# Kernel optimization log

Hardware: AMD Instinct MI355X
Metric: run time of the kernel (lower is better)

## Reference

```python
import jax, jax.numpy as jnp
import numpy as np

N = 4
SEGMENTS = 16
IN_F = 256
OUT_F = 256
BATCH = 512


def chebyshev_lobatto(n):
    # Chebyshev-Lobatto interpolation nodes on [-1, 1]
    k = jnp.arange(n, dtype=jnp.float32)
    return -jnp.cos(jnp.pi * k / (n - 1))


def lagrange_basis(x, nodes):
    # x: [B, In]; returns basis values [B, In, n]
    n = nodes.shape[0]
    cols = []
    for j in range(n):  # n is a small static constant (4)
        terms = [(x - nodes[m]) / (nodes[j] - nodes[m]) for m in range(n) if m != j]
        cols.append(jnp.prod(jnp.stack(terms, axis=0), axis=0))
    return jnp.stack(cols, axis=-1)


def setup_inputs() -> dict:
    key = jax.random.key(0)
    k1, k2 = jax.random.split(key)
    x = jax.random.uniform(k1, (BATCH, IN_F), dtype=jnp.float32, minval=-1.0, maxval=1.0)
    w = jax.random.uniform(
        k2, (OUT_F, IN_F, (N - 1) * SEGMENTS + 1), dtype=jnp.float32, minval=-1.0, maxval=1.0
    )
    return {"x": x, "w": w, "n": N, "segments": SEGMENTS}


def reference(x, w, n, segments):
    nodes = chebyshev_lobatto(n)
    # segment id per element, clamped to [0, segments-1]
    id_min = jnp.clip(((x + 1.0) / 2.0 * segments).astype(jnp.int32), 0, segments - 1)
    id_max = id_min + 1
    wid_min = id_min * (n - 1)  # start of weight slice; slice length == n
    # segment boundaries in x-space: eta(i) = i/segments * 2 - 1
    x_min = id_min.astype(x.dtype) / segments * 2.0 - 1.0
    x_max = id_max.astype(x.dtype) / segments * 2.0 - 1.0
    # rescale x into [-1, 1] within its segment
    x_in = 2.0 * (x - x_min) / (x_max - x_min) - 1.0
    basis = lagrange_basis(x_in, nodes)  # [B, In, n]
    # gather per-element weight slice: w_g[b,i,j,o] = w[o, i, wid_min[b,i]+j]
    idx = wid_min[..., None] + jnp.arange(n)  # [B, In, n]
    w_t = jnp.transpose(w, (1, 2, 0))  # [In, K, Out]
    in_f = w.shape[1]
    w_g = w_t[jnp.arange(in_f)[None, :, None], idx]  # [B, In, n, Out]
    # interpolate and sum over in_features (matches einsum 'ijk,jkli->jl')
    return jnp.einsum("bin,bino->bo", basis, w_g)
```

## Files before the change

kernel.cpp:

```cpp
#include <hip/hip_runtime.h>


typedef _Float16 h2 __attribute__((ext_vector_type(2)));

#define INF     256
#define OUTF    256
#define WSTRIDE 49
#define OSTRIDE (INF * WSTRIDE)
#define NSPLIT  32
#define IPB     8
#define WE_UINTS (256 * 128 * 64)

#define GLOAD16(gptr, lptr)                                                         \
  __builtin_amdgcn_global_load_lds(                                                 \
      (const __attribute__((address_space(1))) unsigned int*)(gptr),                \
      (__attribute__((address_space(3))) unsigned int*)(lptr), 16, 0, 0)

__global__ __launch_bounds__(256)
void pp_expand(const float* __restrict__ w, unsigned int* __restrict__ we) {
    const int i = blockIdx.x;
    const int o = threadIdx.x;
    const float* src = w + (size_t)o * OSTRIDE + i * WSTRIDE;
    float t[49];
    #pragma unroll
    for (int k = 0; k < 49; ++k) t[k] = src[k];
    const int op = o >> 1, e = o & 1;
    unsigned int* dst = we + ((size_t)i * 128 + op) * 64 + e * 2;
    #pragma unroll
    for (int s = 0; s < 16; ++s) {
        auto p0 = __builtin_amdgcn_cvt_pkrtz(t[3*s],   t[3*s+1]);
        auto p1 = __builtin_amdgcn_cvt_pkrtz(t[3*s+2], t[3*s+3]);
        uint2 v;
        v.x = __builtin_bit_cast(unsigned int, p0);
        v.y = __builtin_bit_cast(unsigned int, p1);
        *(uint2*)(dst + s * 4) = v;
    }
}

__global__ __launch_bounds__(256, 4)
void pp_partial(const float* __restrict__ x, const unsigned int* __restrict__ we,
                float* __restrict__ part) {
    __shared__ unsigned int smem[8192];

    const int tid  = threadIdx.x;
    const int wave = tid >> 6, lane = tid & 63;
    const int isplit  = blockIdx.x;
    const int i_base  = isplit * IPB;
    const int op_base = blockIdx.y * 16;
    const int o_base  = blockIdx.y * 32;
    const int b_base  = blockIdx.z * 64;
    const int b = b_base + lane;

    #pragma unroll
    for (int it = 0; it < 8; ++it) {
        int u = it * 256 + tid;
        int iloc = u >> 8, opl = (u >> 4) & 15, s = u & 15;
        const unsigned int* gp =
            we + (((size_t)(i_base + iloc) * 128 + op_base + opl) * 16 + s) * 4;
        GLOAD16(gp, &smem[u * 4]);
    }

    int sseg[IPB]; h2 cA[IPB], cB[IPB];
    {
        const float4* xp = (const float4*)(x + (size_t)b * INF + i_base);
        float4 x0 = xp[0], x1 = xp[1];
        float xs[8] = {x0.x, x0.y, x0.z, x0.w, x1.x, x1.y, x1.z, x1.w};
        #pragma unroll
        for (int i = 0; i < IPB; ++i) {
            float xx = xs[i];
            int id = (int)((xx + 1.0f) * 8.0f);
            id = id < 0 ? 0 : (id > 15 ? 15 : id);
            float u = (xx - ((float)id * 0.125f - 1.0f)) * 16.0f - 1.0f;
            float a = u + 1.0f, b2 = u + 0.5f, cc = u - 0.5f, d = u - 1.0f;
            float c0 = b2 * cc * d  * (-2.0f / 3.0f);
            float c1 = a  * cc * d  * ( 4.0f / 3.0f);
            float c2 = a  * b2 * d  * (-4.0f / 3.0f);
            float c3 = a  * b2 * cc * ( 2.0f / 3.0f);
            h2 pA; pA[0] = (_Float16)c0; pA[1] = (_Float16)c1;
            h2 pB; pB[0] = (_Float16)c2; pB[1] = (_Float16)c3;
            cA[i] = pA; cB[i] = pB; sseg[i] = id;
        }
    }

    __syncthreads();

    float acc[8];
    #pragma unroll
    for (int q = 0; q < 8; ++q) acc[q] = 0.0f;

    #pragma unroll
    for (int i = 0; i < IPB; ++i) {
        const unsigned int* p = &smem[(i * 16 + wave * 4) * 64 + sseg[i] * 4];
        #pragma unroll
        for (int pq = 0; pq < 4; ++pq) {
            uint4 v = *(const uint4*)(p + pq * 64);
            acc[2*pq]   = __builtin_amdgcn_fdot2(__builtin_bit_cast(h2, v.x), cA[i],
                                                 acc[2*pq],   false);
            acc[2*pq]   = __builtin_amdgcn_fdot2(__builtin_bit_cast(h2, v.y), cB[i],
                                                 acc[2*pq],   false);
            acc[2*pq+1] = __builtin_amdgcn_fdot2(__builtin_bit_cast(h2, v.z), cA[i],
                                                 acc[2*pq+1], false);
            acc[2*pq+1] = __builtin_amdgcn_fdot2(__builtin_bit_cast(h2, v.w), cB[i],
                                                 acc[2*pq+1], false);
        }
    }

    __syncthreads();
    float* smf = (float*)smem;
    #pragma unroll
    for (int q = 0; q < 8; ++q)
        smf[lane * 33 + wave * 8 + q] = acc[q];
    __syncthreads();

    const int qo = tid & 7;
    const int g  = tid >> 3;
    #pragma unroll
    for (int r = 0; r < 2; ++r) {
        int b_l = g + 32 * r;
        float4 v;
        v.x = smf[b_l * 33 + qo * 4 + 0];
        v.y = smf[b_l * 33 + qo * 4 + 1];
        v.z = smf[b_l * 33 + qo * 4 + 2];
        v.w = smf[b_l * 33 + qo * 4 + 3];
        *(float4*)(part + (size_t)isplit * (512 * 256)
                        + (size_t)(b_base + b_l) * 256 + o_base + qo * 4) = v;
    }
}

__global__ __launch_bounds__(256)
void pp_reduce(const float* __restrict__ part, float* __restrict__ out) {
    const size_t off4 = (size_t)blockIdx.x * 256 + threadIdx.x;
    const float4* p4 = (const float4*)part;
    float4 s = make_float4(0.f, 0.f, 0.f, 0.f);
    #pragma unroll
    for (int k = 0; k < NSPLIT; ++k) {
        float4 v = p4[(size_t)k * (512 * 64) + off4];
        s.x += v.x; s.y += v.y; s.z += v.z; s.w += v.w;
    }
    ((float4*)out)[off4] = s;
}

extern "C" void kernel_launch(void* const* d_in, const int* in_sizes, int n_in,
                              void* d_out, int out_size, void* d_ws, size_t ws_size,
                              hipStream_t stream) {
    const float* x = (const float*)d_in[0];
    const float* w = (const float*)d_in[1];
    float* out = (float*)d_out;
    unsigned int* we = (unsigned int*)d_ws;
    float* part = (float*)((char*)d_ws + (size_t)WE_UINTS * 4);
    (void)ws_size; (void)n_in; (void)in_sizes; (void)out_size;

    pp_expand<<<dim3(256), 256, 0, stream>>>(w, we);
    pp_partial<<<dim3(NSPLIT, 8, 8), 256, 0, stream>>>(x, we, part);
    pp_reduce<<<dim3(128), 256, 0, stream>>>(part, out);
}
```

Baseline: 86.46 us.

## Stage weight expansion through LDS and halve input split count

The weight-expansion kernel now loads contiguous weight rows for two output columns into LDS with async global-to-LDS copies. It then writes packed fp16 vectors as 16-byte stores, replacing per-thread strided 49-float reads with coalesced loads. Separately, the partial kernel processes 16 input features per block instead of 8, halving the number of partial sums written and reduced, at the cost of double the LDS and lower occupancy (launch bound 2).

```diff
diff --git a/kernel.cpp b/kernel.cpp
--- a/kernel.cpp
+++ b/kernel.cpp
@@ -7,8 +7,8 @@
 #define OUTF    256
 #define WSTRIDE 49
 #define OSTRIDE (INF * WSTRIDE)
-#define NSPLIT  32
-#define IPB     8
+#define NSPLIT  16
+#define IPB     16
 #define WE_UINTS (256 * 128 * 64)
 
 #define GLOAD16(gptr, lptr)                                                         \
@@ -18,29 +18,53 @@
 
 __global__ __launch_bounds__(256)
 void pp_expand(const float* __restrict__ w, unsigned int* __restrict__ we) {
-    const int i = blockIdx.x;
-    const int o = threadIdx.x;
-    const float* src = w + (size_t)o * OSTRIDE + i * WSTRIDE;
-    float t[49];
-    #pragma unroll
-    for (int k = 0; k < 49; ++k) t[k] = src[k];
-    const int op = o >> 1, e = o & 1;
-    unsigned int* dst = we + ((size_t)i * 128 + op) * 64 + e * 2;
-    #pragma unroll
-    for (int s = 0; s < 16; ++s) {
-        auto p0 = __builtin_amdgcn_cvt_pkrtz(t[3*s],   t[3*s+1]);
-        auto p1 = __builtin_amdgcn_cvt_pkrtz(t[3*s+2], t[3*s+3]);
-        uint2 v;
-        v.x = __builtin_bit_cast(unsigned int, p0);
-        v.y = __builtin_bit_cast(unsigned int, p1);
-        *(uint2*)(dst + s * 4) = v;
+    __shared__ float lds_w[2][3136];
+
+    const int tid   = threadIdx.x;
+    const int op    = blockIdx.x >> 1;
+    const int ihalf = blockIdx.x & 1;
+    const int o0    = op * 2;
+
+    for (int c = 0; c < 2; ++c) {
+        const int i_c = ihalf * 128 + c * 64;
+
+        #pragma unroll
+        for (int oe = 0; oe < 2; ++oe) {
+            const float* src = w + (size_t)(o0 + oe) * OSTRIDE + (size_t)i_c * WSTRIDE;
+            #pragma unroll
+            for (int it = 0; it < 4; ++it) {
+                int u = it * 256 + tid;
+                if (u < 784)
+                    GLOAD16(src + u * 4, &lds_w[oe][u * 4]);
+            }
+        }
+        __syncthreads();
+
+        #pragma unroll
+        for (int r = 0; r < 4; ++r) {
+            int item = r * 256 + tid;
+            int il = item >> 4, s = item & 15;
+            const float* t0 = &lds_w[0][il * 49 + 3 * s];
+            const float* t1 = &lds_w[1][il * 49 + 3 * s];
+            uint4 v;
+            v.x = __builtin_bit_cast(unsigned int,
+                      __builtin_amdgcn_cvt_pkrtz(t0[0], t0[1]));
+            v.y = __builtin_bit_cast(unsigned int,
+                      __builtin_amdgcn_cvt_pkrtz(t0[2], t0[3]));
+            v.z = __builtin_bit_cast(unsigned int,
+                      __builtin_amdgcn_cvt_pkrtz(t1[0], t1[1]));
+            v.w = __builtin_bit_cast(unsigned int,
+                      __builtin_amdgcn_cvt_pkrtz(t1[2], t1[3]));
+            *(uint4*)(we + (((size_t)(i_c + il) * 128 + op) * 16 + s) * 4) = v;
+        }
+        __syncthreads();
     }
 }
 
-__global__ __launch_bounds__(256, 4)
+__global__ __launch_bounds__(256, 2)
 void pp_partial(const float* __restrict__ x, const unsigned int* __restrict__ we,
                 float* __restrict__ part) {
-    __shared__ unsigned int smem[8192];
+    __shared__ unsigned int smem[16384];
 
     const int tid  = threadIdx.x;
     const int wave = tid >> 6, lane = tid & 63;
@@ -52,7 +76,7 @@
     const int b = b_base + lane;
 
     #pragma unroll
-    for (int it = 0; it < 8; ++it) {
+    for (int it = 0; it < 16; ++it) {
         int u = it * 256 + tid;
         int iloc = u >> 8, opl = (u >> 4) & 15, s = u & 15;
         const unsigned int* gp =
@@ -63,8 +87,9 @@
     int sseg[IPB]; h2 cA[IPB], cB[IPB];
     {
         const float4* xp = (const float4*)(x + (size_t)b * INF + i_base);
-        float4 x0 = xp[0], x1 = xp[1];
-        float xs[8] = {x0.x, x0.y, x0.z, x0.w, x1.x, x1.y, x1.z, x1.w};
+        float4 x0 = xp[0], x1 = xp[1], x2 = xp[2], x3 = xp[3];
+        float xs[16] = {x0.x, x0.y, x0.z, x0.w, x1.x, x1.y, x1.z, x1.w,
+                        x2.x, x2.y, x2.z, x2.w, x3.x, x3.y, x3.z, x3.w};
         #pragma unroll
         for (int i = 0; i < IPB; ++i) {
             float xx = xs[i];
```

Result: no change. 85.30 us (-1.3%).
